# Performance work log

Hardware: AMD Instinct MI355X
Metric: run time of the kernel (lower is better)

The kernel has to match this reference:

```python
import jax, jax.numpy as jnp
import numpy as np

N_NODES = 50000
N_EDGES = 800000
DIMS = [128, 128, 128, 64]  # in, hid1, hid2, out
EPS = 1e-12


def setup_inputs() -> dict:
    key = jax.random.key(0)
    ks = jax.random.split(key, 32)
    inp = {
        "x": jax.random.normal(ks[0], (N_NODES, DIMS[0]), dtype=jnp.float32),
        "edge_src": jax.random.randint(ks[1], (N_EDGES,), 0, N_NODES),
        "edge_dst": jax.random.randint(ks[2], (N_EDGES,), 0, N_NODES),
    }
    k = 3
    for l in range(3):
        din, dout = DIMS[l], DIMS[l + 1]
        s_in = 1.0 / np.sqrt(din)
        inp[f"Wp{l+1}"] = jax.random.uniform(ks[k], (din, din), jnp.float32, -s_in, s_in); k += 1
        inp[f"bp{l+1}"] = jax.random.uniform(ks[k], (din,), jnp.float32, -s_in, s_in); k += 1
        inp[f"Ws{l+1}"] = jax.random.uniform(ks[k], (din, dout), jnp.float32, -s_in, s_in); k += 1
        inp[f"Wn{l+1}"] = jax.random.uniform(ks[k], (din, dout), jnp.float32, -s_in, s_in); k += 1
        inp[f"b{l+1}"] = jnp.zeros((dout,), jnp.float32); k += 1
    return inp


def _sage_pool_layer(x, src, dst, Wp, bp, Ws, Wn, b):
    # per-edge: relu(fc_pool(x_src)); [E, din]
    m = jax.nn.relu(x[src] @ Wp + bp)
    # max-pool over in-neighbors of each dst node; [N, din]
    pooled = jax.ops.segment_max(m, dst, num_segments=x.shape[0])
    deg = jax.ops.segment_sum(jnp.ones((dst.shape[0],), x.dtype), dst,
                              num_segments=x.shape[0])
    pooled = jnp.where(deg[:, None] > 0, pooled, 0.0)  # zero-degree -> 0 (DGL)
    return x @ Ws + pooled @ Wn + b


def _l2norm_relu(h):
    n = jnp.sqrt(jnp.sum(h * h, axis=1, keepdims=True))
    return jax.nn.relu(h / jnp.maximum(n, EPS))


def reference(x, edge_src, edge_dst,
              Wp1, bp1, Ws1, Wn1, b1,
              Wp2, bp2, Ws2, Wn2, b2,
              Wp3, bp3, Ws3, Wn3, b3):
    h = _l2norm_relu(_sage_pool_layer(x, edge_src, edge_dst, Wp1, bp1, Ws1, Wn1, b1))
    h = _l2norm_relu(_sage_pool_layer(h, edge_src, edge_dst, Wp2, bp2, Ws2, Wn2, b2))
    h = _l2norm_relu(_sage_pool_layer(h, edge_src, edge_dst, Wp3, bp3, Ws3, Wn3, b3))
    return h
```

## Files before the change

### kernel.cpp

```cpp
#include <hip/hip_runtime.h>
#include <math.h>

#define N_NODES 50000
#define N_EDGES 800000
#define DIN 128
#define RANGES 8
#define NODES_PER_RANGE 6250
#define CAP 64

typedef __attribute__((ext_vector_type(8))) short short8;
typedef __attribute__((ext_vector_type(2))) short short2v;
typedef __attribute__((ext_vector_type(4))) float f32x4;

__device__ __forceinline__ unsigned short f2bf(float f) {
    unsigned int u = __float_as_uint(f);
    return (unsigned short)((u + 0x7FFFu + ((u >> 16) & 1u)) >> 16);
}
__device__ __forceinline__ float bf2f(unsigned short h) {
    return __uint_as_float(((unsigned int)h) << 16);
}

struct GSegs { const unsigned short* a[2]; const unsigned short* b[2]; };

template <int NTILES, int NSEG, int OMODE>
__global__ __launch_bounds__(256) void gemm_mfma(
    GSegs segs, const float* __restrict__ bias,
    unsigned short* __restrict__ outH, float* __restrict__ outF, int M)
{
    const int N = NTILES * 16;
    const int lane = threadIdx.x & 63;
    const int wv = threadIdx.x >> 6;
    const int cl = lane & 15;
    const int quad = lane >> 4;
    const int rowBase = blockIdx.x * 64 + wv * 16;

    f32x4 acc[NTILES];
    #pragma unroll
    for (int t = 0; t < NTILES; ++t) acc[t] = (f32x4){0.f, 0.f, 0.f, 0.f};

    const int aBase = (rowBase + cl) * 128 + quad * 8;
    const int bLane = cl * 32 + quad * 8;

    #pragma unroll
    for (int s = 0; s < NSEG; ++s) {
        const unsigned short* __restrict__ A = segs.a[s];
        const unsigned short* __restrict__ B = segs.b[s];
        #pragma unroll
        for (int c = 0; c < 4; ++c) {
            short8 af = *(const short8*)(A + aBase + c * 32);
            const unsigned short* Bc = B + c * (N * 32) + bLane;
            #pragma unroll
            for (int t = 0; t < NTILES; ++t) {
                short8 bf = *(const short8*)(Bc + t * 512);
                acc[t] = __builtin_amdgcn_mfma_f32_16x16x32_bf16(af, bf, acc[t], 0, 0, 0);
            }
        }
    }

    #pragma unroll
    for (int t = 0; t < NTILES; ++t) {
        float bc = bias[t * 16 + cl];
        #pragma unroll
        for (int g = 0; g < 4; ++g) acc[t][g] += bc;
    }

    const int row0 = rowBase + quad * 4;

    if (OMODE == 0) {
        #pragma unroll
        for (int t = 0; t < NTILES; ++t)
            #pragma unroll
            for (int g = 0; g < 4; ++g) {
                int r = row0 + g;
                if (r < M)
                    outH[r * N + t * 16 + cl] = f2bf(fmaxf(acc[t][g], 0.0f));
            }
        return;
    }

    float inv[4];
    #pragma unroll
    for (int g = 0; g < 4; ++g) {
        float s = 0.f;
        #pragma unroll
        for (int t = 0; t < NTILES; ++t) s += acc[t][g] * acc[t][g];
        s += __shfl_xor(s, 1, 64);
        s += __shfl_xor(s, 2, 64);
        s += __shfl_xor(s, 4, 64);
        s += __shfl_xor(s, 8, 64);
        inv[g] = 1.0f / fmaxf(sqrtf(s), 1e-12f);
    }

    #pragma unroll
    for (int t = 0; t < NTILES; ++t)
        #pragma unroll
        for (int g = 0; g < 4; ++g) {
            int r = row0 + g;
            if (r >= M) continue;
            float o = fmaxf(acc[t][g] * inv[g], 0.0f);
            int off = r * N + t * 16 + cl;
            if (OMODE == 1) outH[off] = f2bf(o);
            else            outF[off] = o;
        }
}

struct WDesc { const float* W; int N; };
struct WDescs { WDesc d[9]; };

__global__ __launch_bounds__(256) void convert_weights(WDescs wd, unsigned short* base)
{
    int mi = blockIdx.y;
    int id = blockIdx.x * 256 + threadIdx.x;
    const float* W = wd.d[mi].W;
    int N = wd.d[mi].N;
    if (id >= 128 * N) return;
    int c = id / (N * 32);
    int n = (id - c * N * 32) >> 5;
    int k = c * 32 + (id & 31);
    base[mi * 16384 + id] = f2bf(W[k * N + n]);
}

__global__ __launch_bounds__(256) void convert_x(
    const float* __restrict__ x, unsigned short* __restrict__ xh)
{
    int i = blockIdx.x * 256 + threadIdx.x;
    float2 v = ((const float2*)x)[i];
    ushort2 h;
    h.x = f2bf(v.x);
    h.y = f2bf(v.y);
    ((ushort2*)xh)[i] = h;
}

__global__ __launch_bounds__(256) void csr_fill_range(
    const int* __restrict__ src, const int* __restrict__ dst,
    int* __restrict__ deg, unsigned short* __restrict__ csr16)
{
    int range = blockIdx.x & (RANGES - 1);
    int e = (blockIdx.x >> 3) * 256 + threadIdx.x;
    int d = dst[e];
    if ((unsigned)(d - range * NODES_PER_RANGE) >= (unsigned)NODES_PER_RANGE) return;
    int r = atomicAdd(&deg[d], 1);
    if (r < CAP) csr16[(d << 6) + r] = (unsigned short)src[e];
}

__global__ __launch_bounds__(256) void pool_max8(
    const unsigned short* __restrict__ y, const int* __restrict__ deg,
    const unsigned short* __restrict__ csr16, unsigned short* __restrict__ pool)
{
    const int wv = threadIdx.x >> 6;
    const int d = threadIdx.x & 63;
    const int n = blockIdx.x * 4 + wv;
    const int e0 = n << 6;
    const int e1 = e0 + min(deg[n], CAP);
    const unsigned short* yb = y + 2 * d;

    short2v acc = (short2v){0, 0};
    int e = e0;
    for (; e + 8 <= e1; e += 8) {
        int s0 = csr16[e + 0], s1 = csr16[e + 1];
        int s2 = csr16[e + 2], s3 = csr16[e + 3];
        int s4 = csr16[e + 4], s5 = csr16[e + 5];
        int s6 = csr16[e + 6], s7 = csr16[e + 7];
        short2v v0 = *(const short2v*)(yb + (s0 << 7));
        short2v v1 = *(const short2v*)(yb + (s1 << 7));
        short2v v2 = *(const short2v*)(yb + (s2 << 7));
        short2v v3 = *(const short2v*)(yb + (s3 << 7));
        short2v v4 = *(const short2v*)(yb + (s4 << 7));
        short2v v5 = *(const short2v*)(yb + (s5 << 7));
        short2v v6 = *(const short2v*)(yb + (s6 << 7));
        short2v v7 = *(const short2v*)(yb + (s7 << 7));
        acc = __builtin_elementwise_max(acc, v0);
        acc = __builtin_elementwise_max(acc, v1);
        acc = __builtin_elementwise_max(acc, v2);
        acc = __builtin_elementwise_max(acc, v3);
        acc = __builtin_elementwise_max(acc, v4);
        acc = __builtin_elementwise_max(acc, v5);
        acc = __builtin_elementwise_max(acc, v6);
        acc = __builtin_elementwise_max(acc, v7);
    }
    for (; e < e1; ++e) {
        int s = csr16[e];
        short2v v = *(const short2v*)(yb + (s << 7));
        acc = __builtin_elementwise_max(acc, v);
    }
    *(short2v*)(pool + n * DIN + 2 * d) = acc;
}

extern "C" void kernel_launch(void* const* d_in, const int* in_sizes, int n_in,
                              void* d_out, int out_size, void* d_ws, size_t ws_size,
                              hipStream_t stream) {
    const float* x    = (const float*)d_in[0];
    const int*   esrc = (const int*)d_in[1];
    const int*   edst = (const int*)d_in[2];
    const float* Wp[3], *bp[3], *Ws[3], *Wn[3], *bb[3];
    for (int l = 0; l < 3; ++l) {
        Wp[l] = (const float*)d_in[3 + 5 * l];
        bp[l] = (const float*)d_in[4 + 5 * l];
        Ws[l] = (const float*)d_in[5 + 5 * l];
        Wn[l] = (const float*)d_in[6 + 5 * l];
        bb[l] = (const float*)d_in[7 + 5 * l];
    }

    const int NF = N_NODES * DIN;
    unsigned short* Y   = (unsigned short*)d_ws;
    unsigned short* PL  = Y + NF;
    unsigned short* Xh  = PL + NF;
    unsigned short* H1  = Xh + NF;
    unsigned short* Wpk = H1 + NF;
    int* deg = (int*)(Wpk + 9 * 16384);
    unsigned short* csr16 = (unsigned short*)(deg + N_NODES);

    auto WH = [&](int i) { return Wpk + i * 16384; };

    const dim3 blk(256);
    const int edgeBlocks = N_EDGES / 256;
    const int gemmBlocks = (N_NODES + 63) / 64;
    const int poolBlocks = N_NODES / 4;

    WDescs wd;
    wd.d[0] = {Wp[0], 128}; wd.d[1] = {Ws[0], 128}; wd.d[2] = {Wn[0], 128};
    wd.d[3] = {Wp[1], 128}; wd.d[4] = {Ws[1], 128}; wd.d[5] = {Wn[1], 128};
    wd.d[6] = {Wp[2], 128}; wd.d[7] = {Ws[2], 64};  wd.d[8] = {Wn[2], 64};
    convert_weights<<<dim3(64, 9), blk, 0, stream>>>(wd, Wpk);
    convert_x<<<NF / 512, blk, 0, stream>>>(x, Xh);
    hipMemsetAsync(deg, 0, N_NODES * sizeof(int), stream);
    csr_fill_range<<<edgeBlocks * RANGES, blk, 0, stream>>>(esrc, edst, deg, csr16);

    GSegs s1, s2;

    s1.a[0] = Xh; s1.b[0] = WH(0);
    gemm_mfma<8, 1, 0><<<gemmBlocks, blk, 0, stream>>>(s1, bp[0], Y, nullptr, N_NODES);
    pool_max8<<<poolBlocks, blk, 0, stream>>>(Y, deg, csr16, PL);
    s2.a[0] = Xh; s2.b[0] = WH(1);
    s2.a[1] = PL; s2.b[1] = WH(2);
    gemm_mfma<8, 2, 1><<<gemmBlocks, blk, 0, stream>>>(s2, bb[0], H1, nullptr, N_NODES);

    s1.a[0] = H1; s1.b[0] = WH(3);
    gemm_mfma<8, 1, 0><<<gemmBlocks, blk, 0, stream>>>(s1, bp[1], Y, nullptr, N_NODES);
    pool_max8<<<poolBlocks, blk, 0, stream>>>(Y, deg, csr16, PL);
    s2.a[0] = H1; s2.b[0] = WH(4);
    s2.a[1] = PL; s2.b[1] = WH(5);
    gemm_mfma<8, 2, 1><<<gemmBlocks, blk, 0, stream>>>(s2, bb[1], Xh, nullptr, N_NODES);

    s1.a[0] = Xh; s1.b[0] = WH(6);
    gemm_mfma<8, 1, 0><<<gemmBlocks, blk, 0, stream>>>(s1, bp[2], Y, nullptr, N_NODES);
    pool_max8<<<poolBlocks, blk, 0, stream>>>(Y, deg, csr16, PL);
    s2.a[0] = Xh; s2.b[0] = WH(7);
    s2.a[1] = PL; s2.b[1] = WH(8);
    gemm_mfma<4, 2, 2><<<gemmBlocks, blk, 0, stream>>>(s2, bb[2], nullptr, (float*)d_out, N_NODES);
}
```

Baseline: 355.5 us.

## Fuse pooling, combine GEMM and next-layer pool GEMM into one per-layer kernel

```diff
diff --git a/kernel.cpp b/kernel.cpp
--- a/kernel.cpp
+++ b/kernel.cpp
@@ -3,10 +3,12 @@
 
 #define N_NODES 50000
 #define N_EDGES 800000
-#define DIN 128
+#define CAP 64
 #define RANGES 8
 #define NODES_PER_RANGE 6250
-#define CAP 64
+#define CSRB 1024
+#define GEMMB 782
+#define LROW 136
 
 typedef __attribute__((ext_vector_type(8))) short short8;
 typedef __attribute__((ext_vector_type(2))) short short2v;
@@ -16,66 +18,190 @@
     unsigned int u = __float_as_uint(f);
     return (unsigned short)((u + 0x7FFFu + ((u >> 16) & 1u)) >> 16);
 }
-__device__ __forceinline__ float bf2f(unsigned short h) {
-    return __uint_as_float(((unsigned int)h) << 16);
-}
-
-struct GSegs { const unsigned short* a[2]; const unsigned short* b[2]; };
-
-template <int NTILES, int NSEG, int OMODE>
-__global__ __launch_bounds__(256) void gemm_mfma(
-    GSegs segs, const float* __restrict__ bias,
-    unsigned short* __restrict__ outH, float* __restrict__ outF, int M)
+
+template <bool F32>
+__device__ __forceinline__ short8 loadA(const void* A, int off) {
+    short8 r;
+    if (F32) {
+        const float* p = (const float*)A + off;
+        float4 f0 = *(const float4*)p;
+        float4 f1 = *(const float4*)(p + 4);
+        r[0] = (short)f2bf(f0.x); r[1] = (short)f2bf(f0.y);
+        r[2] = (short)f2bf(f0.z); r[3] = (short)f2bf(f0.w);
+        r[4] = (short)f2bf(f1.x); r[5] = (short)f2bf(f1.y);
+        r[6] = (short)f2bf(f1.z); r[7] = (short)f2bf(f1.w);
+    } else {
+        r = *(const short8*)((const unsigned short*)A + off);
+    }
+    return r;
+}
+
+struct WDescs { const float* W[9]; int N[9]; };
+
+__global__ __launch_bounds__(256) void prep_kernel(
+    WDescs wd, unsigned short* __restrict__ Wpk, int* __restrict__ deg)
 {
-    const int N = NTILES * 16;
+    const int nthr = gridDim.x * 256;
+    const int tid = blockIdx.x * 256 + threadIdx.x;
+    for (int id = tid; id < 9 * 16384; id += nthr) {
+        int mi = id >> 14;
+        int loc = id & 16383;
+        int N = wd.N[mi];
+        if (loc < 128 * N) {
+            int c = loc / (N * 32);
+            int n = (loc - c * N * 32) >> 5;
+            int k = c * 32 + (loc & 31);
+            Wpk[mi * 16384 + loc] = f2bf(wd.W[mi][k * N + n]);
+        }
+    }
+    for (int i = tid; i < N_NODES; i += nthr) deg[i] = 0;
+}
+
+__global__ __launch_bounds__(256) void mix_kernel(
+    const int* __restrict__ esrc, const int* __restrict__ edst,
+    int* __restrict__ deg, unsigned short* __restrict__ csr16,
+    const float* __restrict__ x, const unsigned short* __restrict__ Wp1,
+    const float* __restrict__ bp1, unsigned short* __restrict__ Y)
+{
+    if (blockIdx.x < CSRB) {
+        int range = blockIdx.x & (RANGES - 1);
+        for (int cb = blockIdx.x >> 3; cb < N_EDGES / 256; cb += CSRB / 8) {
+            int e = cb * 256 + threadIdx.x;
+            int d = edst[e];
+            if ((unsigned)(d - range * NODES_PER_RANGE) < (unsigned)NODES_PER_RANGE) {
+                int r = atomicAdd(&deg[d], 1);
+                if (r < CAP) csr16[(d << 6) + r] = (unsigned short)esrc[e];
+            }
+        }
+        return;
+    }
+    const int tile = blockIdx.x - CSRB;
     const int lane = threadIdx.x & 63;
     const int wv = threadIdx.x >> 6;
     const int cl = lane & 15;
     const int quad = lane >> 4;
-    const int rowBase = blockIdx.x * 64 + wv * 16;
-
-    f32x4 acc[NTILES];
-    #pragma unroll
-    for (int t = 0; t < NTILES; ++t) acc[t] = (f32x4){0.f, 0.f, 0.f, 0.f};
-
-    const int aBase = (rowBase + cl) * 128 + quad * 8;
+    const int rowBase = tile * 64 + wv * 16;
+    const int ar = min(rowBase + cl, N_NODES - 1);
     const int bLane = cl * 32 + quad * 8;
 
-    #pragma unroll
-    for (int s = 0; s < NSEG; ++s) {
-        const unsigned short* __restrict__ A = segs.a[s];
-        const unsigned short* __restrict__ B = segs.b[s];
-        #pragma unroll
-        for (int c = 0; c < 4; ++c) {
-            short8 af = *(const short8*)(A + aBase + c * 32);
-            const unsigned short* Bc = B + c * (N * 32) + bLane;
-            #pragma unroll
-            for (int t = 0; t < NTILES; ++t) {
-                short8 bf = *(const short8*)(Bc + t * 512);
-                acc[t] = __builtin_amdgcn_mfma_f32_16x16x32_bf16(af, bf, acc[t], 0, 0, 0);
+    f32x4 acc[8];
+    #pragma unroll
+    for (int t = 0; t < 8; ++t) acc[t] = (f32x4){0.f, 0.f, 0.f, 0.f};
+
+    #pragma unroll
+    for (int c = 0; c < 4; ++c) {
+        short8 af = loadA<true>(x, ar * 128 + c * 32 + quad * 8);
+        const unsigned short* Bc = Wp1 + c * 4096 + bLane;
+        #pragma unroll
+        for (int t = 0; t < 8; ++t) {
+            short8 bf = *(const short8*)(Bc + t * 512);
+            acc[t] = __builtin_amdgcn_mfma_f32_16x16x32_bf16(af, bf, acc[t], 0, 0, 0);
+        }
+    }
+    const int row0 = rowBase + quad * 4;
+    #pragma unroll
+    for (int t = 0; t < 8; ++t) {
+        float bc = bp1[t * 16 + cl];
+        #pragma unroll
+        for (int g = 0; g < 4; ++g) {
+            int r = row0 + g;
+            if (r < N_NODES)
+                Y[r * 128 + t * 16 + cl] = f2bf(fmaxf(acc[t][g] + bc, 0.0f));
+        }
+    }
+}
+
+template <bool A0F32, bool LAST>
+__global__ __launch_bounds__(256) void pd_kernel(
+    const void* __restrict__ A0,
+    const unsigned short* __restrict__ B0, const unsigned short* __restrict__ B1,
+    const float* __restrict__ bias,
+    const unsigned short* __restrict__ Yin, const int* __restrict__ deg,
+    const unsigned short* __restrict__ csr16,
+    unsigned short* __restrict__ outH, float* __restrict__ outF,
+    const unsigned short* __restrict__ Bnext, const float* __restrict__ bnext,
+    unsigned short* __restrict__ Yout)
+{
+    constexpr int NT = LAST ? 4 : 8;
+    constexpr int N = NT * 16;
+    __shared__ unsigned short lds[4][16 * LROW];
+
+    const int lane = threadIdx.x & 63;
+    const int wv = threadIdx.x >> 6;
+    const int cl = lane & 15;
+    const int quad = lane >> 4;
+    const int tile = blockIdx.x;
+    const int nodeBase = tile * 64 + wv * 16;
+    unsigned short* plw = &lds[wv][0];
+
+    {
+        const unsigned short* yb = Yin + 2 * lane;
+        for (int j = 0; j < 16; ++j) {
+            int n = min(nodeBase + j, N_NODES - 1);
+            int e0 = n << 6;
+            int e1 = e0 + min(deg[n], CAP);
+            short2v acc = (short2v){0, 0};
+            int e = e0;
+            for (; e + 8 <= e1; e += 8) {
+                int s0 = csr16[e + 0], s1 = csr16[e + 1];
+                int s2 = csr16[e + 2], s3 = csr16[e + 3];
+                int s4 = csr16[e + 4], s5 = csr16[e + 5];
+                int s6 = csr16[e + 6], s7 = csr16[e + 7];
+                short2v v0 = *(const short2v*)(yb + (s0 << 7));
+                short2v v1 = *(const short2v*)(yb + (s1 << 7));
+                short2v v2 = *(const short2v*)(yb + (s2 << 7));
+                short2v v3 = *(const short2v*)(yb + (s3 << 7));
+                short2v v4 = *(const short2v*)(yb + (s4 << 7));
+                short2v v5 = *(const short2v*)(yb + (s5 << 7));
+                short2v v6 = *(const short2v*)(yb + (s6 << 7));
+                short2v v7 = *(const short2v*)(yb + (s7 << 7));
+                acc = __builtin_elementwise_max(acc, v0);
+                acc = __builtin_elementwise_max(acc, v1);
+                acc = __builtin_elementwise_max(acc, v2);
+                acc = __builtin_elementwise_max(acc, v3);
+                acc = __builtin_elementwise_max(acc, v4);
+                acc = __builtin_elementwise_max(acc, v5);
+                acc = __builtin_elementwise_max(acc, v6);
+                acc = __builtin_elementwise_max(acc, v7);
             }
-        }
-    }
-
-    #pragma unroll
-    for (int t = 0; t < NTILES; ++t) {
+            for (; e < e1; ++e) {
+                int s = csr16[e];
+                short2v v = *(const short2v*)(yb + (s << 7));
+                acc = __builtin_elementwise_max(acc, v);
+            }
+            *(short2v*)(plw + j * LROW + 2 * lane) = acc;
+        }
+    }
+
+    const int ar = min(nodeBase + cl, N_NODES - 1);
+    const int bLane = cl * 32 + quad * 8;
+    f32x4 acc[NT];
+    #pragma unroll
+    for (int t = 0; t < NT; ++t) acc[t] = (f32x4){0.f, 0.f, 0.f, 0.f};
+
+    #pragma unroll
+    for (int c = 0; c < 4; ++c) {
+        short8 a0 = loadA<A0F32>(A0, ar * 128 + c * 32 + quad * 8);
+        short8 a1 = *(const short8*)(plw + cl * LROW + c * 32 + quad * 8);
+        const unsigned short* B0c = B0 + c * (N * 32) + bLane;
+        const unsigned short* B1c = B1 + c * (N * 32) + bLane;
+        #pragma unroll
+        for (int t = 0; t < NT; ++t) {
+            short8 bf = *(const short8*)(B0c + t * 512);
+            acc[t] = __builtin_amdgcn_mfma_f32_16x16x32_bf16(a0, bf, acc[t], 0, 0, 0);
+        }
+        #pragma unroll
+        for (int t = 0; t < NT; ++t) {
+            short8 bf = *(const short8*)(B1c + t * 512);
+            acc[t] = __builtin_amdgcn_mfma_f32_16x16x32_bf16(a1, bf, acc[t], 0, 0, 0);
+        }
+    }
+
+    #pragma unroll
+    for (int t = 0; t < NT; ++t) {
         float bc = bias[t * 16 + cl];
         #pragma unroll
         for (int g = 0; g < 4; ++g) acc[t][g] += bc;
-    }
-
-    const int row0 = rowBase + quad * 4;
-
-    if (OMODE == 0) {
-        #pragma unroll
-        for (int t = 0; t < NTILES; ++t)
-            #pragma unroll
-            for (int g = 0; g < 4; ++g) {
-                int r = row0 + g;
-                if (r < M)
-                    outH[r * N + t * 16 + cl] = f2bf(fmaxf(acc[t][g], 0.0f));
-            }
-        return;
     }
 
     float inv[4];
@@ -83,7 +209,7 @@
     for (int g = 0; g < 4; ++g) {
         float s = 0.f;
         #pragma unroll
-        for (int t = 0; t < NTILES; ++t) s += acc[t][g] * acc[t][g];
+        for (int t = 0; t < NT; ++t) s += acc[t][g] * acc[t][g];
         s += __shfl_xor(s, 1, 64);
         s += __shfl_xor(s, 2, 64);
         s += __shfl_xor(s, 4, 64);
@@ -91,99 +217,53 @@
         inv[g] = 1.0f / fmaxf(sqrtf(s), 1e-12f);
     }
 
-    #pragma unroll
-    for (int t = 0; t < NTILES; ++t)
+    const int row0 = nodeBase + quad * 4;
+
+    if (LAST) {
+        #pragma unroll
+        for (int t = 0; t < NT; ++t)
+            #pragma unroll
+            for (int g = 0; g < 4; ++g) {
+                int r = row0 + g;
+                if (r < N_NODES)
+                    outF[r * N + t * 16 + cl] = fmaxf(acc[t][g] * inv[g], 0.0f);
+            }
+        return;
+    }
+
+    #pragma unroll
+    for (int t = 0; t < NT; ++t)
         #pragma unroll
         for (int g = 0; g < 4; ++g) {
             int r = row0 + g;
-            if (r >= M) continue;
-            float o = fmaxf(acc[t][g] * inv[g], 0.0f);
-            int off = r * N + t * 16 + cl;
-            if (OMODE == 1) outH[off] = f2bf(o);
-            else            outF[off] = o;
-        }
-}
-
-struct WDesc { const float* W; int N; };
-struct WDescs { WDesc d[9]; };
-
-__global__ __launch_bounds__(256) void convert_weights(WDescs wd, unsigned short* base)
-{
-    int mi = blockIdx.y;
-    int id = blockIdx.x * 256 + threadIdx.x;
-    const float* W = wd.d[mi].W;
-    int N = wd.d[mi].N;
-    if (id >= 128 * N) return;
-    int c = id / (N * 32);
-    int n = (id - c * N * 32) >> 5;
-    int k = c * 32 + (id & 31);
-    base[mi * 16384 + id] = f2bf(W[k * N + n]);
-}
-
-__global__ __launch_bounds__(256) void convert_x(
-    const float* __restrict__ x, unsigned short* __restrict__ xh)
-{
-    int i = blockIdx.x * 256 + threadIdx.x;
-    float2 v = ((const float2*)x)[i];
-    ushort2 h;
-    h.x = f2bf(v.x);
-    h.y = f2bf(v.y);
-    ((ushort2*)xh)[i] = h;
-}
-
-__global__ __launch_bounds__(256) void csr_fill_range(
-    const int* __restrict__ src, const int* __restrict__ dst,
-    int* __restrict__ deg, unsigned short* __restrict__ csr16)
-{
-    int range = blockIdx.x & (RANGES - 1);
-    int e = (blockIdx.x >> 3) * 256 + threadIdx.x;
-    int d = dst[e];
-    if ((unsigned)(d - range * NODES_PER_RANGE) >= (unsigned)NODES_PER_RANGE) return;
-    int r = atomicAdd(&deg[d], 1);
-    if (r < CAP) csr16[(d << 6) + r] = (unsigned short)src[e];
-}
-
-__global__ __launch_bounds__(256) void pool_max8(
-    const unsigned short* __restrict__ y, const int* __restrict__ deg,
-    const unsigned short* __restrict__ csr16, unsigned short* __restrict__ pool)
-{
-    const int wv = threadIdx.x >> 6;
-    const int d = threadIdx.x & 63;
-    const int n = blockIdx.x * 4 + wv;
-    const int e0 = n << 6;
-    const int e1 = e0 + min(deg[n], CAP);
-    const unsigned short* yb = y + 2 * d;
-
-    short2v acc = (short2v){0, 0};
-    int e = e0;
-    for (; e + 8 <= e1; e += 8) {
-        int s0 = csr16[e + 0], s1 = csr16[e + 1];
-        int s2 = csr16[e + 2], s3 = csr16[e + 3];
-        int s4 = csr16[e + 4], s5 = csr16[e + 5];
-        int s6 = csr16[e + 6], s7 = csr16[e + 7];
-        short2v v0 = *(const short2v*)(yb + (s0 << 7));
-        short2v v1 = *(const short2v*)(yb + (s1 << 7));
-        short2v v2 = *(const short2v*)(yb + (s2 << 7));
-        short2v v3 = *(const short2v*)(yb + (s3 << 7));
-        short2v v4 = *(const short2v*)(yb + (s4 << 7));
-        short2v v5 = *(const short2v*)(yb + (s5 << 7));
-        short2v v6 = *(const short2v*)(yb + (s6 << 7));
-        short2v v7 = *(const short2v*)(yb + (s7 << 7));
-        acc = __builtin_elementwise_max(acc, v0);
-        acc = __builtin_elementwise_max(acc, v1);
-        acc = __builtin_elementwise_max(acc, v2);
-        acc = __builtin_elementwise_max(acc, v3);
-        acc = __builtin_elementwise_max(acc, v4);
-        acc = __builtin_elementwise_max(acc, v5);
-        acc = __builtin_elementwise_max(acc, v6);
-        acc = __builtin_elementwise_max(acc, v7);
-    }
-    for (; e < e1; ++e) {
-        int s = csr16[e];
-        short2v v = *(const short2v*)(yb + (s << 7));
-        acc = __builtin_elementwise_max(acc, v);
-    }
-    *(short2v*)(pool + n * DIN + 2 * d) = acc;
+            unsigned short h = f2bf(fmaxf(acc[t][g] * inv[g], 0.0f));
+            if (r < N_NODES) outH[r * 128 + t * 16 + cl] = h;
+            plw[(quad * 4 + g) * LROW + t * 16 + cl] = h;
+        }
+
+    f32x4 ya[8];
+    #pragma unroll
+    for (int t = 0; t < 8; ++t) ya[t] = (f32x4){0.f, 0.f, 0.f, 0.f};
+    #pragma unroll
+    for (int c = 0; c < 4; ++c) {
+        short8 af = *(const short8*)(plw + cl * LROW + c * 32 + quad * 8);
+        const unsigned short* Bc = Bnext + c * 4096 + bLane;
+        #pragma unroll
+        for (int t = 0; t < 8; ++t) {
+            short8 bf = *(const short8*)(Bc + t * 512);
+            ya[t] = __builtin_amdgcn_mfma_f32_16x16x32_bf16(af, bf, ya[t], 0, 0, 0);
+        }
+    }
+    #pragma unroll
+    for (int t = 0; t < 8; ++t) {
+        float bc = bnext[t * 16 + cl];
+        #pragma unroll
+        for (int g = 0; g < 4; ++g) {
+            int r = row0 + g;
+            if (r < N_NODES)
+                Yout[r * 128 + t * 16 + cl] = f2bf(fmaxf(ya[t][g] + bc, 0.0f));
+        }
+    }
 }
 
 extern "C" void kernel_launch(void* const* d_in, const int* in_sizes, int n_in,
@@ -201,51 +281,36 @@
         bb[l] = (const float*)d_in[7 + 5 * l];
     }
 
-    const int NF = N_NODES * DIN;
-    unsigned short* Y   = (unsigned short*)d_ws;
-    unsigned short* PL  = Y + NF;
-    unsigned short* Xh  = PL + NF;
-    unsigned short* H1  = Xh + NF;
-    unsigned short* Wpk = H1 + NF;
+    const int NF = N_NODES * 128;
+    unsigned short* YA  = (unsigned short*)d_ws;
+    unsigned short* YB  = YA + NF;
+    unsigned short* H1  = YB + NF;
+    unsigned short* H2  = H1 + NF;
+    unsigned short* Wpk = H2 + NF;
     int* deg = (int*)(Wpk + 9 * 16384);
     unsigned short* csr16 = (unsigned short*)(deg + N_NODES);
 
     auto WH = [&](int i) { return Wpk + i * 16384; };
 
-    const dim3 blk(256);
-    const int edgeBlocks = N_EDGES / 256;
-    const int gemmBlocks = (N_NODES + 63) / 64;
-    const int poolBlocks = N_NODES / 4;
-
     WDescs wd;
-    wd.d[0] = {Wp[0], 128}; wd.d[1] = {Ws[0], 128}; wd.d[2] = {Wn[0], 128};
-    wd.d[3] = {Wp[1], 128}; wd.d[4] = {Ws[1], 128}; wd.d[5] = {Wn[1], 128};
-    wd.d[6] = {Wp[2], 128}; wd.d[7] = {Ws[2], 64};  wd.d[8] = {Wn[2], 64};
-    convert_weights<<<dim3(64, 9), blk, 0, stream>>>(wd, Wpk);
-    convert_x<<<NF / 512, blk, 0, stream>>>(x, Xh);
-    hipMemsetAsync(deg, 0, N_NODES * sizeof(int), stream);
-    csr_fill_range<<<edgeBlocks * RANGES, blk, 0, stream>>>(esrc, edst, deg, csr16);
-
-    GSegs s1, s2;
-
-    s1.a[0] = Xh; s1.b[0] = WH(0);
-    gemm_mfma<8, 1, 0><<<gemmBlocks, blk, 0, stream>>>(s1, bp[0], Y, nullptr, N_NODES);
-    pool_max8<<<poolBlocks, blk, 0, stream>>>(Y, deg, csr16, PL);
-    s2.a[0] = Xh; s2.b[0] = WH(1);
-    s2.a[1] = PL; s2.b[1] = WH(2);
-    gemm_mfma<8, 2, 1><<<gemmBlocks, blk, 0, stream>>>(s2, bb[0], H1, nullptr, N_NODES);
-
-    s1.a[0] = H1; s1.b[0] = WH(3);
-    gemm_mfma<8, 1, 0><<<gemmBlocks, blk, 0, stream>>>(s1, bp[1], Y, nullptr, N_NODES);
-    pool_max8<<<poolBlocks, blk, 0, stream>>>(Y, deg, csr16, PL);
-    s2.a[0] = H1; s2.b[0] = WH(4);
-    s2.a[1] = PL; s2.b[1] = WH(5);
-    gemm_mfma<8, 2, 1><<<gemmBlocks, blk, 0, stream>>>(s2, bb[1], Xh, nullptr, N_NODES);
-
-    s1.a[0] = Xh; s1.b[0] = WH(6);
-    gemm_mfma<8, 1, 0><<<gemmBlocks, blk, 0, stream>>>(s1, bp[2], Y, nullptr, N_NODES);
-    pool_max8<<<poolBlocks, blk, 0, stream>>>(Y, deg, csr16, PL);
-    s2.a[0] = Xh; s2.b[0] = WH(7);
-    s2.a[1] = PL; s2.b[1] = WH(8);
-    gemm_mfma<4, 2, 2><<<gemmBlocks, blk, 0, stream>>>(s2, bb[2], nullptr, (float*)d_out, N_NODES);
-}
+    wd.W[0] = Wp[0]; wd.N[0] = 128;
+    wd.W[1] = Ws[0]; wd.N[1] = 128;
+    wd.W[2] = Wn[0]; wd.N[2] = 128;
+    wd.W[3] = Wp[1]; wd.N[3] = 128;
+    wd.W[4] = Ws[1]; wd.N[4] = 128;
+    wd.W[5] = Wn[1]; wd.N[5] = 128;
+    wd.W[6] = Wp[2]; wd.N[6] = 128;
+    wd.W[7] = Ws[2]; wd.N[7] = 64;
+    wd.W[8] = Wn[2]; wd.N[8] = 64;
+
+    prep_kernel<<<576, 256, 0, stream>>>(wd, Wpk, deg);
+    mix_kernel<<<CSRB + GEMMB, 256, 0, stream>>>(esrc, edst, deg, csr16,
+                                                 x, WH(0), bp[0], YA);
+    pd_kernel<true, false><<<GEMMB, 256, 0, stream>>>(
+        x, WH(1), WH(2), bb[0], YA, deg, csr16, H1, nullptr, WH(3), bp[1], YB);
+    pd_kernel<false, false><<<GEMMB, 256, 0, stream>>>(
+        H1, WH(4), WH(5), bb[1], YB, deg, csr16, H2, nullptr, WH(6), bp[2], YA);
+    pd_kernel<false, true><<<GEMMB, 256, 0, stream>>>(
+        H2, WH(7), WH(8), bb[2], YA, deg, csr16, nullptr, (float*)d_out,
+        nullptr, nullptr, nullptr);
+}
```

After: 390.8 us. 9.9% more time.
